# Kernel optimization log

Hardware: AMD Instinct MI355X
Metric: run time of the kernel (lower is better)

The kernel has to match this reference:

```python
import jax, jax.numpy as jnp
from jax import lax
import numpy as np

BATCH, T, IN_DIM, RES = 32, 2048, 64, 1024
SPECTRAL_RADIUS, SPARSITY, INPUT_SCALING, LEAK = 1.2, 0.2, 0.5, 0.3


def setup_inputs() -> dict:
    key = jax.random.key(0)
    inputs = jax.random.normal(key, (BATCH, T, IN_DIM), dtype=jnp.float32)
    # Replicate the layer's build(): fixed random reservoir, seeded numpy RNG.
    rng = np.random.RandomState(42)
    W_in = rng.uniform(-INPUT_SCALING, INPUT_SCALING, size=(IN_DIM, RES)).astype(np.float32)
    W_res = rng.randn(RES, RES)
    mask = rng.rand(RES, RES) < SPARSITY
    W_res *= mask
    sr = np.max(np.abs(np.linalg.eigvals(W_res)))
    if sr > 0:
        W_res *= SPECTRAL_RADIUS / sr
    return {
        "inputs": inputs,
        "W_in": jnp.asarray(W_in),
        "W_res": jnp.asarray(W_res.astype(np.float32)),
    }


def reference(inputs, W_in, W_res):
    # inputs: [B, T, I]; W_in: [I, R]; W_res: [R, R]
    leak = jnp.asarray(LEAK, inputs.dtype)
    # Hoist the input projection out of the recurrence (same math, one big GEMM).
    x_proj = jnp.einsum("bti,ir->btr", inputs, W_in)  # [B, T, R]
    state0 = jnp.zeros((inputs.shape[0], W_res.shape[0]), dtype=inputs.dtype)

    def step(state, x_t):  # x_t: [B, R]
        new_state = jnp.tanh(x_t + state @ W_res)
        state = (1.0 - leak) * state + leak * new_state
        return state, state

    _, states = lax.scan(step, state0, jnp.swapaxes(x_proj, 0, 1))  # [T, B, R]
    return jnp.swapaxes(states, 0, 1)  # [B, T, R] (return_sequences=True)
```

## Files before the change

kernel.cpp:

```cpp
#include <hip/hip_runtime.h>

#define T_STEPS 2048
#define NBATCH  32
#define IN_DIM  64
#define RES     1024
#define LEAKF   0.3f

__global__ __launch_bounds__(256) void esn_step(
    const float* __restrict__ inp,
    const float* __restrict__ Win,
    const float* __restrict__ Wres,
    float* __restrict__ out,
    float* __restrict__ sT,
    int t)
{
    const int tid   = threadIdx.x;
    const int c_loc = tid & 15;
    const int ks    = tid >> 4;
    const int c0    = blockIdx.x * 16;
    const int b0    = blockIdx.y * 8;
    const int c     = c0 + c_loc;

    const float* sTr = sT + ((t & 1) ^ 1) * (RES * NBATCH);
    float*       sTw = sT + (t & 1) * (RES * NBATCH);

    float acc0 = 0.f, acc1 = 0.f, acc2 = 0.f, acc3 = 0.f;
    float acc4 = 0.f, acc5 = 0.f, acc6 = 0.f, acc7 = 0.f;

    if (t > 0) {
        const int kbeg = ks * 64;
        const float* wp = Wres + (size_t)kbeg * RES + c;
        const float* sp = sTr + kbeg * NBATCH + b0;
        #pragma unroll 4
        for (int j = 0; j < 64; ++j) {
            const float w = wp[(size_t)j * RES];
            const float4 sa = *reinterpret_cast<const float4*>(sp + j * NBATCH);
            const float4 sb = *reinterpret_cast<const float4*>(sp + j * NBATCH + 4);
            acc0 = fmaf(sa.x, w, acc0);
            acc1 = fmaf(sa.y, w, acc1);
            acc2 = fmaf(sa.z, w, acc2);
            acc3 = fmaf(sa.w, w, acc3);
            acc4 = fmaf(sb.x, w, acc4);
            acc5 = fmaf(sb.y, w, acc5);
            acc6 = fmaf(sb.z, w, acc6);
            acc7 = fmaf(sb.w, w, acc7);
        }
    }

    __shared__ float pl[16][8][17];
    pl[ks][0][c_loc] = acc0;
    pl[ks][1][c_loc] = acc1;
    pl[ks][2][c_loc] = acc2;
    pl[ks][3][c_loc] = acc3;
    pl[ks][4][c_loc] = acc4;
    pl[ks][5][c_loc] = acc5;
    pl[ks][6][c_loc] = acc6;
    pl[ks][7][c_loc] = acc7;
    __syncthreads();

    if (tid < 128) {
        const int b  = tid >> 4;
        const int cl = tid & 15;
        const int cg = c0 + cl;
        const int bg = b0 + b;

        float sum = 0.f;
        #pragma unroll
        for (int q = 0; q < 16; ++q) sum += pl[q][b][cl];

        const float* inb = inp + ((size_t)bg * T_STEPS + t) * IN_DIM;
        float x = 0.f;
        #pragma unroll 8
        for (int i = 0; i < IN_DIM; ++i)
            x = fmaf(inb[i], Win[(size_t)i * RES + cg], x);

        const float a  = x + sum;
        const float nw = tanhf(a);
        const float spv = (t > 0) ? sTr[cg * NBATCH + bg] : 0.f;
        const float sn = fmaf(1.0f - LEAKF, spv, LEAKF * nw);

        out[((size_t)bg * T_STEPS + t) * RES + cg] = sn;
        sTw[cg * NBATCH + bg] = sn;
    }
}

extern "C" void kernel_launch(void* const* d_in, const int* in_sizes, int n_in,
                              void* d_out, int out_size, void* d_ws, size_t ws_size,
                              hipStream_t stream)
{
    const float* inp  = (const float*)d_in[0];
    const float* Win  = (const float*)d_in[1];
    const float* Wres = (const float*)d_in[2];
    float* out = (float*)d_out;
    float* sT  = (float*)d_ws;

    dim3 grid(64, 4);
    dim3 blk(256);
    for (int t = 0; t < T_STEPS; ++t) {
        hipLaunchKernelGGL(esn_step, grid, blk, 0, stream,
                           inp, Win, Wres, out, sT, t);
    }
}
```

Before: 20.53 ms.

## Replace per-step launches with persistent kernel using flag-based inter-block sync

Launches one persistent kernel of 256 blocks that loops over all time steps, instead of 2048 separate launches. Each block keeps its slice of W_res in registers and keeps its previous state in a register. Blocks in the same batch group wait on per-block step counters in global memory before reading the shared state. This removes per-step launch overhead and repeated weight reloads. In exchange it relies on all blocks being co-resident, and it uses relaxed atomics without acquire/release fences, so the ordering between state writes and flag updates may not be guaranteed.

```diff
diff --git a/kernel.cpp b/kernel.cpp
--- a/kernel.cpp
+++ b/kernel.cpp
@@ -5,6 +5,118 @@
 #define IN_DIM  64
 #define RES     1024
 #define LEAKF   0.3f
+#define NCG     64
+#define NBG     4
+
+typedef unsigned long long u64cp;
+
+__global__ __launch_bounds__(256, 1) void esn_persist(
+    const float* __restrict__ inp,
+    const float* __restrict__ Win,
+    const float* __restrict__ Wres,
+    float* __restrict__ out,
+    float* __restrict__ sT,
+    unsigned* __restrict__ flags)
+{
+    const int tid   = threadIdx.x;
+    const int c_loc = tid & 15;
+    const int ks    = tid >> 4;
+    const int cg    = blockIdx.x;
+    const int bg    = blockIdx.y;
+    const int c0    = cg * 16;
+    const int b0    = bg * 8;
+    const int c     = c0 + c_loc;
+
+    float w[64];
+    {
+        const float* wp = Wres + (size_t)(ks * 64) * RES + c;
+        #pragma unroll
+        for (int j = 0; j < 64; ++j) w[j] = wp[(size_t)j * RES];
+    }
+
+    __shared__ float pl[16][8][17];
+    unsigned* flg = flags + bg * NCG;
+
+    const int fb = tid >> 4;
+    float s_prev = 0.f;
+
+    for (int t = 0; t < T_STEPS; ++t) {
+        float* sTr = sT + ((t & 1) ^ 1) * (RES * NBATCH);
+        float* sTw = sT + (t & 1) * (RES * NBATCH);
+
+        float x = 0.f;
+        if (tid < 128) {
+            const float* inb = inp + ((size_t)(b0 + fb) * T_STEPS + t) * IN_DIM;
+            #pragma unroll 8
+            for (int i = 0; i < IN_DIM; ++i)
+                x = fmaf(inb[i], Win[(size_t)i * RES + c], x);
+        }
+
+        if (t > 0) {
+            if (tid < NCG) {
+                const unsigned tgt = (unsigned)t;
+                while (__hip_atomic_load(&flg[tid], __ATOMIC_RELAXED,
+                                         __HIP_MEMORY_SCOPE_AGENT) < tgt) { }
+            }
+            __syncthreads();
+        }
+
+        float acc0 = 0.f, acc1 = 0.f, acc2 = 0.f, acc3 = 0.f;
+        float acc4 = 0.f, acc5 = 0.f, acc6 = 0.f, acc7 = 0.f;
+        if (t > 0) {
+            float* sp = sTr + (size_t)(ks * 64) * NBATCH + b0;
+            #pragma unroll
+            for (int j = 0; j < 64; ++j) {
+                u64cp p01 = __hip_atomic_load((u64cp*)(sp + (size_t)j * NBATCH + 0),
+                                              __ATOMIC_RELAXED, __HIP_MEMORY_SCOPE_AGENT);
+                u64cp p23 = __hip_atomic_load((u64cp*)(sp + (size_t)j * NBATCH + 2),
+                                              __ATOMIC_RELAXED, __HIP_MEMORY_SCOPE_AGENT);
+                u64cp p45 = __hip_atomic_load((u64cp*)(sp + (size_t)j * NBATCH + 4),
+                                              __ATOMIC_RELAXED, __HIP_MEMORY_SCOPE_AGENT);
+                u64cp p67 = __hip_atomic_load((u64cp*)(sp + (size_t)j * NBATCH + 6),
+                                              __ATOMIC_RELAXED, __HIP_MEMORY_SCOPE_AGENT);
+                const float wj = w[j];
+                acc0 = fmaf(__uint_as_float((unsigned)(p01       )), wj, acc0);
+                acc1 = fmaf(__uint_as_float((unsigned)(p01 >> 32u)), wj, acc1);
+                acc2 = fmaf(__uint_as_float((unsigned)(p23       )), wj, acc2);
+                acc3 = fmaf(__uint_as_float((unsigned)(p23 >> 32u)), wj, acc3);
+                acc4 = fmaf(__uint_as_float((unsigned)(p45       )), wj, acc4);
+                acc5 = fmaf(__uint_as_float((unsigned)(p45 >> 32u)), wj, acc5);
+                acc6 = fmaf(__uint_as_float((unsigned)(p67       )), wj, acc6);
+                acc7 = fmaf(__uint_as_float((unsigned)(p67 >> 32u)), wj, acc7);
+            }
+        }
+
+        pl[ks][0][c_loc] = acc0;
+        pl[ks][1][c_loc] = acc1;
+        pl[ks][2][c_loc] = acc2;
+        pl[ks][3][c_loc] = acc3;
+        pl[ks][4][c_loc] = acc4;
+        pl[ks][5][c_loc] = acc5;
+        pl[ks][6][c_loc] = acc6;
+        pl[ks][7][c_loc] = acc7;
+        __syncthreads();
+
+        if (tid < 128) {
+            float sum = 0.f;
+            #pragma unroll
+            for (int q = 0; q < 16; ++q) sum += pl[q][fb][c_loc];
+
+            const float nw = tanhf(x + sum);
+            const float sn = fmaf(1.0f - LEAKF, s_prev, LEAKF * nw);
+            s_prev = sn;
+
+            out[((size_t)(b0 + fb) * T_STEPS + t) * RES + c] = sn;
+            __hip_atomic_store(sTw + (size_t)c * NBATCH + (b0 + fb), sn,
+                               __ATOMIC_RELAXED, __HIP_MEMORY_SCOPE_AGENT);
+        }
+        __syncthreads();
+
+        if (tid == 0)
+            __hip_atomic_store(&flg[cg], (unsigned)(t + 1),
+                               __ATOMIC_RELAXED, __HIP_MEMORY_SCOPE_AGENT);
+    }
+}
 
 __global__ __launch_bounds__(256) void esn_step(
     const float* __restrict__ inp,
@@ -94,8 +206,18 @@
     float* out = (float*)d_out;
     float* sT  = (float*)d_ws;
 
-    dim3 grid(64, 4);
-    dim3 blk(256);
+    const size_t stateBytes = (size_t)2 * RES * NBATCH * sizeof(float);
+    const size_t flagBytes  = (size_t)NBG * NCG * sizeof(unsigned);
+
+    if (ws_size >= stateBytes + flagBytes) {
+        unsigned* flags = (unsigned*)((char*)d_ws + stateBytes);
+        hipMemsetAsync(flags, 0, flagBytes, stream);
+        hipLaunchKernelGGL(esn_persist, dim3(NCG, NBG), dim3(256), 0, stream,
+                           inp, Win, Wres, out, sT, flags);
+        return;
+    }
+
+    dim3 grid(64, 4), blk(256);
     for (int t = 0; t < T_STEPS; ++t) {
         hipLaunchKernelGGL(esn_step, grid, blk, 0, stream,
                            inp, Win, Wres, out, sT, t);
```

Result: no change. 20.23 ms (-1.5%).
